# Optimization experiments

Hardware: AMD Instinct MI355X
Metric: run time of the kernel (lower is better)

Reference implementation:

```python
import jax, jax.numpy as jnp
import numpy as np

N = 100000          # nodes
E = 1600000         # edges (before self-loops)
F_IN = 128          # raw node features
TOPO = 8            # topological feature dim
HEADS1, HID1 = 8, 8 # conv1: 8 heads x 8 channels, concat -> 64
C_OUT = 40          # classes (conv2: 1 head, no concat)
NEG_SLOPE = 0.2     # PyG GATConv leaky_relu slope


def setup_inputs() -> dict:
    key = jax.random.key(0)
    ks = jax.random.split(key, 12)
    x = jax.random.normal(ks[0], (N, F_IN), jnp.float32)
    topo = jax.random.normal(ks[1], (N, TOPO), jnp.float32)
    edge_index = jax.random.randint(ks[2], (2, E), 0, N, jnp.int32)
    s = 0.1
    W1 = jax.random.normal(ks[3], (F_IN + TOPO, HEADS1 * HID1), jnp.float32) * s
    a_src1 = jax.random.normal(ks[4], (HEADS1, HID1), jnp.float32) * s
    a_dst1 = jax.random.normal(ks[5], (HEADS1, HID1), jnp.float32) * s
    b1 = jnp.zeros((HEADS1 * HID1,), jnp.float32)
    W2 = jax.random.normal(ks[6], (HEADS1 * HID1, C_OUT), jnp.float32) * s
    a_src2 = jax.random.normal(ks[7], (1, C_OUT), jnp.float32) * s
    a_dst2 = jax.random.normal(ks[8], (1, C_OUT), jnp.float32) * s
    b2 = jnp.zeros((C_OUT,), jnp.float32)
    return {"x": x, "topo": topo, "edge_index": edge_index,
            "W1": W1, "a_src1": a_src1, "a_dst1": a_dst1, "b1": b1,
            "W2": W2, "a_src2": a_src2, "a_dst2": a_dst2, "b2": b2}


def _gat_conv(x, src, dst, W, a_src, a_dst, b, heads, concat):
    # x: [N, Fin]; src/dst: [Etot] (self-loops already included)
    n = x.shape[0]
    h = (x @ W).reshape(n, heads, -1)                 # [N, H, C]
    alpha_s = jnp.sum(h * a_src[None], axis=-1)       # [N, H]
    alpha_d = jnp.sum(h * a_dst[None], axis=-1)       # [N, H]
    e = jax.nn.leaky_relu(alpha_s[src] + alpha_d[dst], NEG_SLOPE)  # [Etot, H]
    # segment softmax over destination nodes (numerically stable)
    m = jax.ops.segment_max(e, dst, num_segments=n)   # [N, H]
    ex = jnp.exp(e - m[dst])
    z = jax.ops.segment_sum(ex, dst, num_segments=n)  # [N, H]
    alpha = ex / (z[dst] + 1e-16)                     # [Etot, H]
    out = jax.ops.segment_sum(h[src] * alpha[..., None], dst, num_segments=n)  # [N,H,C]
    out = out.reshape(n, -1) if concat else out.mean(axis=1)
    return out + b


def reference(x, topo, edge_index, W1, a_src1, a_dst1, b1, W2, a_src2, a_dst2, b2):
    n = x.shape[0]
    loops = jnp.arange(n, dtype=edge_index.dtype)
    src = jnp.concatenate([edge_index[0], loops])  # PyG add_self_loops=True
    dst = jnp.concatenate([edge_index[1], loops])
    h = jnp.concatenate([x, topo], axis=1)         # [N, F_IN + TOPO]
    # dropout is identity in eval mode
    h = jax.nn.elu(_gat_conv(h, src, dst, W1, a_src1, a_dst1, b1, HEADS1, True))
    logits = _gat_conv(h, src, dst, W2, a_src2, a_dst2, b2, 1, False)
    return jax.nn.log_softmax(logits, axis=1)
```

## Files before the change

kernel.cpp:

```cpp
#include <hip/hip_runtime.h>
#include <math.h>


#define NBUK_MAX 512
#define BIN_CHUNK 4096
#define BUK_CAP 4608

typedef unsigned short ushort_t;

__device__ inline unsigned int f2bf(float f) {
    unsigned int u = __float_as_uint(f);
    u += 0x7FFFu + ((u >> 16) & 1u);
    return u >> 16;
}
__device__ inline float bf_lo(unsigned int u) {
    return __uint_as_float(u << 16);
}
__device__ inline float bf_hi(unsigned int u) {
    return __uint_as_float(u & 0xFFFF0000u);
}
__device__ inline float lrelu_exp(float q) {
    return __expf(q >= 0.f ? q : 0.2f * q);
}

__device__ inline int wave_incl_scan(int v, int lane) {
    #pragma unroll
    for (int ofs = 1; ofs < 64; ofs <<= 1) {
        int t = __shfl_up(v, ofs);
        if (lane >= ofs) v += t;
    }
    return v;
}

__global__ __launch_bounds__(256) void k_bin(const int* __restrict__ src,
                                             const int* __restrict__ dst,
                                             int* __restrict__ gCursor,
                                             unsigned int* __restrict__ tmp,
                                             int E, int NBUK) {
    __shared__ int lcnt[NBUK_MAX];
    __shared__ int lcur[NBUK_MAX];
    int tid = threadIdx.x;
    int base = blockIdx.x * BIN_CHUNK;
    for (int i = tid; i < NBUK; i += 256) lcnt[i] = 0;
    __syncthreads();
    int d[16];
    #pragma unroll
    for (int q = 0; q < 4; q++) {
        int e = base + q * 1024 + 4 * tid;
        if (e + 3 < E) {
            int4 v = *(const int4*)&dst[e];
            d[4 * q + 0] = v.x; d[4 * q + 1] = v.y;
            d[4 * q + 2] = v.z; d[4 * q + 3] = v.w;
        } else {
            #pragma unroll
            for (int k = 0; k < 4; k++)
                d[4 * q + k] = (e + k < E) ? dst[e + k] : -1;
        }
    }
    #pragma unroll
    for (int k = 0; k < 16; k++)
        if (d[k] >= 0) atomicAdd(&lcnt[d[k] >> 8], 1);
    __syncthreads();
    for (int b = tid; b < NBUK; b += 256) {
        int c = lcnt[b];
        lcur[b] = c ? b * BUK_CAP + atomicAdd(&gCursor[b], c) : 0;
    }
    __syncthreads();
    #pragma unroll
    for (int q = 0; q < 4; q++) {
        int e = base + q * 1024 + 4 * tid;
        int s[4];
        if (e + 3 < E) {
            int4 v = *(const int4*)&src[e];
            s[0] = v.x; s[1] = v.y; s[2] = v.z; s[3] = v.w;
        } else {
            #pragma unroll
            for (int k = 0; k < 4; k++)
                s[k] = (e + k < E) ? src[e + k] : 0;
        }
        #pragma unroll
        for (int k = 0; k < 4; k++) {
            int dd = d[4 * q + k];
            if (dd >= 0) {
                int p = atomicAdd(&lcur[dd >> 8], 1);
                tmp[p] = ((unsigned int)s[k] << 8) | (unsigned int)(dd & 255);
            }
        }
    }
}

__global__ __launch_bounds__(512) void k_fill2(const unsigned int* __restrict__ tmp,
                                               const int* __restrict__ gCursor,
                                               int* __restrict__ rowptr,
                                               int* __restrict__ rowEnd,
                                               int* __restrict__ csr, int N) {
    __shared__ int cnt[256];
    __shared__ int cur[256];
    __shared__ int wsum[4];
    int b = blockIdx.x, tid = threadIdx.x;
    int e0 = b * BUK_CAP;
    int cnt_e = gCursor[b];
    int e1 = e0 + cnt_e;
    if (tid < 256) cnt[tid] = 0;
    __syncthreads();
    {
        int nq = cnt_e >> 2;
        const uint4* t4 = (const uint4*)(tmp + e0);
        for (int q = tid; q < nq; q += 512) {
            uint4 v = t4[q];
            atomicAdd(&cnt[v.x & 255u], 1);
            atomicAdd(&cnt[v.y & 255u], 1);
            atomicAdd(&cnt[v.z & 255u], 1);
            atomicAdd(&cnt[v.w & 255u], 1);
        }
        for (int i = (nq << 2) + tid; i < cnt_e; i += 512)
            atomicAdd(&cnt[tmp[e0 + i] & 255u], 1);
    }
    __syncthreads();
    if (tid < 256) {
        int lane = tid & 63, wv = tid >> 6;
        int v = cnt[tid];
        int incl = wave_incl_scan(v, lane);
        if (lane == 63) wsum[wv] = incl;
        cnt[tid] = incl - v;
    }
    __syncthreads();
    if (tid < 256) {
        int wv = tid >> 6;
        int woff = 0;
        for (int i = 0; i < wv; i++) woff += wsum[i];
        int excl = woff + cnt[tid];
        int node = b * 256 + tid;
        int start = e0 + excl;
        cur[tid] = start;
        if (node < N) {
            rowptr[node] = start;
        }
    }
    __syncthreads();
    if (tid < 256) {
        int node = b * 256 + tid;
        if (node < N) rowEnd[node] = (tid < 255) ? cur[tid + 1] : e1;
    }
    __syncthreads();
    for (int i = e0 + tid; i < e1; i += 512) {
        unsigned int t = tmp[i];
        int p = atomicAdd(&cur[t & 255u], 1);
        csr[p] = (int)(t >> 8);
    }
}

__global__ __launch_bounds__(256) void k_xform1(const float* __restrict__ x,
                                                const float* __restrict__ topo,
                                                const float* __restrict__ W1,
                                                const float* __restrict__ asrc,
                                                const float* __restrict__ adst,
                                                ushort_t* __restrict__ h1b,
                                                float* __restrict__ as1,
                                                float* __restrict__ ad1, int N) {
    __shared__ float XT[136 * 64];
    __shared__ float WS[136 * 64];
    int tid = threadIdx.x;
    int n0 = blockIdx.x * 64;
    {
        const float4* W4 = (const float4*)W1;
        float4* WS4 = (float4*)WS;
        for (int i = tid; i < 2176; i += 256) WS4[i] = W4[i];
    }
    {
        const float4* x4 = (const float4*)x;
        for (int i = tid; i < 2048; i += 256) {
            int node = i & 63, k4 = i >> 6;
            int gn = n0 + node; if (gn > N - 1) gn = N - 1;
            float4 v = x4[(size_t)gn * 32 + k4];
            int k = k4 * 4;
            XT[(k + 0) * 64 + node] = v.x;
            XT[(k + 1) * 64 + node] = v.y;
            XT[(k + 2) * 64 + node] = v.z;
            XT[(k + 3) * 64 + node] = v.w;
        }
        const float4* t4 = (const float4*)topo;
        if (tid < 128) {
            int node = tid & 63, j4 = tid >> 6;
            int gn = n0 + node; if (gn > N - 1) gn = N - 1;
            float4 v = t4[(size_t)gn * 2 + j4];
            int k = 128 + j4 * 4;
            XT[(k + 0) * 64 + node] = v.x;
            XT[(k + 1) * 64 + node] = v.y;
            XT[(k + 2) * 64 + node] = v.z;
            XT[(k + 3) * 64 + node] = v.w;
        }
    }
    __syncthreads();
    int ci = tid & 15, ni = tid >> 4;
    int nb = ni * 4, cb = ci * 4;
    float acc[16];
    #pragma unroll
    for (int i = 0; i < 16; i++) acc[i] = 0.f;
    #pragma unroll 4
    for (int k = 0; k < 136; k++) {
        float4 xv = *(const float4*)&XT[k * 64 + nb];
        float4 wv = *(const float4*)&WS[k * 64 + cb];
        acc[0]  = fmaf(xv.x, wv.x, acc[0]);  acc[1]  = fmaf(xv.x, wv.y, acc[1]);
        acc[2]  = fmaf(xv.x, wv.z, acc[2]);  acc[3]  = fmaf(xv.x, wv.w, acc[3]);
        acc[4]  = fmaf(xv.y, wv.x, acc[4]);  acc[5]  = fmaf(xv.y, wv.y, acc[5]);
        acc[6]  = fmaf(xv.y, wv.z, acc[6]);  acc[7]  = fmaf(xv.y, wv.w, acc[7]);
        acc[8]  = fmaf(xv.z, wv.x, acc[8]);  acc[9]  = fmaf(xv.z, wv.y, acc[9]);
        acc[10] = fmaf(xv.z, wv.z, acc[10]); acc[11] = fmaf(xv.z, wv.w, acc[11]);
        acc[12] = fmaf(xv.w, wv.x, acc[12]); acc[13] = fmaf(xv.w, wv.y, acc[13]);
        acc[14] = fmaf(xv.w, wv.z, acc[14]); acc[15] = fmaf(xv.w, wv.w, acc[15]);
    }
    int head = cb >> 3;
    #pragma unroll
    for (int i = 0; i < 4; i++) {
        int n = n0 + nb + i;
        unsigned int p0 = f2bf(acc[i * 4 + 0]) | (f2bf(acc[i * 4 + 1]) << 16);
        unsigned int p1 = f2bf(acc[i * 4 + 2]) | (f2bf(acc[i * 4 + 3]) << 16);
        if (n < N) *(uint2*)&h1b[(size_t)n * 64 + cb] = make_uint2(p0, p1);
        float s = 0.f, d = 0.f;
        #pragma unroll
        for (int j = 0; j < 4; j++) {
            s = fmaf(acc[i * 4 + j], asrc[cb + j], s);
            d = fmaf(acc[i * 4 + j], adst[cb + j], d);
        }
        s += __shfl_xor(s, 1);
        d += __shfl_xor(d, 1);
        if ((ci & 1) == 0 && n < N) {
            as1[n * 8 + head] = s;
            ad1[n * 8 + head] = d;
        }
    }
}

#define AGG_FMA(W_, U_)                                           \
    {                                                             \
        acc[0] = fmaf(W_, bf_lo(U_.x), acc[0]);                   \
        acc[1] = fmaf(W_, bf_hi(U_.x), acc[1]);                   \
        acc[2] = fmaf(W_, bf_lo(U_.y), acc[2]);                   \
        acc[3] = fmaf(W_, bf_hi(U_.y), acc[3]);                   \
        acc[4] = fmaf(W_, bf_lo(U_.z), acc[4]);                   \
        acc[5] = fmaf(W_, bf_hi(U_.z), acc[5]);                   \
        acc[6] = fmaf(W_, bf_lo(U_.w), acc[6]);                   \
        acc[7] = fmaf(W_, bf_hi(U_.w), acc[7]);                   \
        z += W_;                                                  \
    }

__global__ __launch_bounds__(256) void k_agg1(const ushort_t* __restrict__ h1b,
                                              const float* __restrict__ as1,
                                              const float* __restrict__ ad1,
                                              const float* __restrict__ b1,
                                              const int* __restrict__ rowptr,
                                              const int* __restrict__ rowEnd,
                                              const int* __restrict__ csr,
                                              float* __restrict__ h2, int N) {
    int tid = threadIdx.x, lane = tid & 63;
    int n = blockIdx.x * 4 + (tid >> 6);
    if (n >= N) return;
    int g = lane >> 3;
    int head = lane & 7;
    const char* h1c = (const char*)h1b;
    unsigned hoff = (unsigned)head << 4;
    float adv = ad1[n * 8 + head];
    float acc[8];
    #pragma unroll
    for (int k = 0; k < 8; k++) acc[k] = 0.f;
    float z = 0.f;
    {
        float w = lrelu_exp(as1[n * 8 + head] + adv);
        if (g == 0) {
            uint4 u = *(const uint4*)(h1c + (((unsigned)n << 7) + hoff));
            acc[0] = w * bf_lo(u.x); acc[1] = w * bf_hi(u.x);
            acc[2] = w * bf_lo(u.y); acc[3] = w * bf_hi(u.y);
            acc[4] = w * bf_lo(u.z); acc[5] = w * bf_hi(u.z);
            acc[6] = w * bf_lo(u.w); acc[7] = w * bf_hi(u.w);
            z = w;
        }
    }
    int j = rowptr[n], j1 = rowEnd[n];
    for (; j + 16 <= j1; j += 16) {
        int cv = csr[j + (lane & 15)];
        int se0 = __shfl(cv, g);
        int se1 = __shfl(cv, 8 + g);
        float av0 = as1[se0 * 8 + head];
        float av1 = as1[se1 * 8 + head];
        uint4 u0 = *(const uint4*)(h1c + (((unsigned)se0 << 7) + hoff));
        uint4 u1 = *(const uint4*)(h1c + (((unsigned)se1 << 7) + hoff));
        float w0 = lrelu_exp(av0 + adv);
        float w1 = lrelu_exp(av1 + adv);
        AGG_FMA(w0, u0);
        AGG_FMA(w1, u1);
    }
    if (j + 8 <= j1) {
        int cv = csr[j + (lane & 7)];
        int se = __shfl(cv, g);
        float av = as1[se * 8 + head];
        uint4 u = *(const uint4*)(h1c + (((unsigned)se << 7) + hoff));
        float w = lrelu_exp(av + adv);
        AGG_FMA(w, u);
        j += 8;
    }
    int t = j1 - j;
    if (t > 0) {
        int idx = (lane & 7); idx = idx < t ? idx : t - 1;
        int cv = csr[j + idx];
        int ge = g < t ? g : t - 1;
        int se = __shfl(cv, ge);
        float w = (g < t) ? lrelu_exp(as1[se * 8 + head] + adv) : 0.f;
        uint4 u = *(const uint4*)(h1c + (((unsigned)se << 7) + hoff));
        AGG_FMA(w, u);
    }
    #pragma unroll
    for (int k = 0; k < 8; k++) {
        acc[k] += __shfl_xor(acc[k], 8);
        acc[k] += __shfl_xor(acc[k], 16);
        acc[k] += __shfl_xor(acc[k], 32);
    }
    z += __shfl_xor(z, 8); z += __shfl_xor(z, 16); z += __shfl_xor(z, 32);
    if (g == 0) {
        float inv = 1.f / (z + 1e-16f);
        float o[8];
        #pragma unroll
        for (int k = 0; k < 8; k++) {
            float v = acc[k] * inv + b1[head * 8 + k];
            o[k] = v > 0.f ? v : (__expf(v) - 1.f);
        }
        float4* dp = (float4*)&h2[(size_t)n * 64 + head * 8];
        dp[0] = make_float4(o[0], o[1], o[2], o[3]);
        dp[1] = make_float4(o[4], o[5], o[6], o[7]);
    }
}

__global__ __launch_bounds__(256) void k_xform2(const float* __restrict__ h2,
                                                const float* __restrict__ W2,
                                                const float* __restrict__ asrc2,
                                                const float* __restrict__ adst2,
                                                ushort_t* __restrict__ gb,
                                                float* __restrict__ as2,
                                                float* __restrict__ ad2, int N) {
    __shared__ float XT[64 * 64];
    __shared__ float WS[64 * 40];
    int tid = threadIdx.x;
    int n0 = blockIdx.x * 64;
    {
        const float4* W4 = (const float4*)W2;
        float4* WS4 = (float4*)WS;
        for (int i = tid; i < 640; i += 256) WS4[i] = W4[i];
    }
    {
        const float4* h4 = (const float4*)h2;
        for (int i = tid; i < 1024; i += 256) {
            int node = i & 63, k4 = i >> 6;
            int gn = n0 + node; if (gn > N - 1) gn = N - 1;
            float4 v = h4[(size_t)gn * 16 + k4];
            int k = k4 * 4;
            XT[(k + 0) * 64 + node] = v.x;
            XT[(k + 1) * 64 + node] = v.y;
            XT[(k + 2) * 64 + node] = v.z;
            XT[(k + 3) * 64 + node] = v.w;
        }
    }
    __syncthreads();
    int ci = tid & 15, ni = tid >> 4;
    int nb = ni * 4, cb = ci * 4;
    float acc[16];
    #pragma unroll
    for (int i = 0; i < 16; i++) acc[i] = 0.f;
    if (ci < 10) {
        #pragma unroll 4
        for (int k = 0; k < 64; k++) {
            float4 xv = *(const float4*)&XT[k * 64 + nb];
            float4 wv = *(const float4*)&WS[k * 40 + cb];
            acc[0]  = fmaf(xv.x, wv.x, acc[0]);  acc[1]  = fmaf(xv.x, wv.y, acc[1]);
            acc[2]  = fmaf(xv.x, wv.z, acc[2]);  acc[3]  = fmaf(xv.x, wv.w, acc[3]);
            acc[4]  = fmaf(xv.y, wv.x, acc[4]);  acc[5]  = fmaf(xv.y, wv.y, acc[5]);
            acc[6]  = fmaf(xv.y, wv.z, acc[6]);  acc[7]  = fmaf(xv.y, wv.w, acc[7]);
            acc[8]  = fmaf(xv.z, wv.x, acc[8]);  acc[9]  = fmaf(xv.z, wv.y, acc[9]);
            acc[10] = fmaf(xv.z, wv.z, acc[10]); acc[11] = fmaf(xv.z, wv.w, acc[11]);
            acc[12] = fmaf(xv.w, wv.x, acc[12]); acc[13] = fmaf(xv.w, wv.y, acc[13]);
            acc[14] = fmaf(xv.w, wv.z, acc[14]); acc[15] = fmaf(xv.w, wv.w, acc[15]);
        }
    }
    #pragma unroll
    for (int i = 0; i < 4; i++) {
        int n = n0 + nb + i;
        if (ci < 10 && n < N) {
            unsigned int p0 = f2bf(acc[i * 4 + 0]) | (f2bf(acc[i * 4 + 1]) << 16);
            unsigned int p1 = f2bf(acc[i * 4 + 2]) | (f2bf(acc[i * 4 + 3]) << 16);
            *(uint2*)&gb[(size_t)n * 64 + cb] = make_uint2(p0, p1);
        }
        float s = 0.f, d = 0.f;
        if (ci < 10) {
            #pragma unroll
            for (int j = 0; j < 4; j++) {
                s = fmaf(acc[i * 4 + j], asrc2[cb + j], s);
                d = fmaf(acc[i * 4 + j], adst2[cb + j], d);
            }
        }
        s += __shfl_xor(s, 1); s += __shfl_xor(s, 2);
        s += __shfl_xor(s, 4); s += __shfl_xor(s, 8);
        d += __shfl_xor(d, 1); d += __shfl_xor(d, 2);
        d += __shfl_xor(d, 4); d += __shfl_xor(d, 8);
        if (ci == 0 && n < N) { as2[n] = s; ad2[n] = d; }
    }
}

__global__ __launch_bounds__(256) void k_agg2(const ushort_t* __restrict__ gb,
                                              const float* __restrict__ as2,
                                              const float* __restrict__ ad2,
                                              const float* __restrict__ b2,
                                              const int* __restrict__ rowptr,
                                              const int* __restrict__ rowEnd,
                                              const int* __restrict__ csr,
                                              float* __restrict__ out, int N) {
    int tid = threadIdx.x, lane = tid & 63;
    int n = blockIdx.x * 4 + (tid >> 6);
    if (n >= N) return;
    int g = lane >> 3;
    int p = lane & 7;
    const char* gbc = (const char*)gb;
    unsigned poff = (unsigned)p << 4;
    float add = ad2[n];
    float acc[8];
    #pragma unroll
    for (int k = 0; k < 8; k++) acc[k] = 0.f;
    float z = 0.f;
    {
        float w = lrelu_exp(as2[n] + add);
        if (g == 0) {
            uint4 u = *(const uint4*)(gbc + (((unsigned)n << 7) + poff));
            acc[0] = w * bf_lo(u.x); acc[1] = w * bf_hi(u.x);
            acc[2] = w * bf_lo(u.y); acc[3] = w * bf_hi(u.y);
            acc[4] = w * bf_lo(u.z); acc[5] = w * bf_hi(u.z);
            acc[6] = w * bf_lo(u.w); acc[7] = w * bf_hi(u.w);
            z = w;
        }
    }
    int j = rowptr[n], j1 = rowEnd[n];
    for (; j + 16 <= j1; j += 16) {
        int cv = csr[j + (lane & 15)];
        int se0 = __shfl(cv, g);
        int se1 = __shfl(cv, 8 + g);
        float av0 = as2[se0];
        float av1 = as2[se1];
        uint4 u0 = *(const uint4*)(gbc + (((unsigned)se0 << 7) + poff));
        uint4 u1 = *(const uint4*)(gbc + (((unsigned)se1 << 7) + poff));
        float w0 = lrelu_exp(av0 + add);
        float w1 = lrelu_exp(av1 + add);
        AGG_FMA(w0, u0);
        AGG_FMA(w1, u1);
    }
    if (j + 8 <= j1) {
        int cv = csr[j + (lane & 7)];
        int se = __shfl(cv, g);
        float av = as2[se];
        uint4 u = *(const uint4*)(gbc + (((unsigned)se << 7) + poff));
        float w = lrelu_exp(av + add);
        AGG_FMA(w, u);
        j += 8;
    }
    int t = j1 - j;
    if (t > 0) {
        int idx = (lane & 7); idx = idx < t ? idx : t - 1;
        int cv = csr[j + idx];
        int ge = g < t ? g : t - 1;
        int se = __shfl(cv, ge);
        float w = (g < t) ? lrelu_exp(as2[se] + add) : 0.f;
        uint4 u = *(const uint4*)(gbc + (((unsigned)se << 7) + poff));
        AGG_FMA(w, u);
    }
    #pragma unroll
    for (int k = 0; k < 8; k++) {
        acc[k] += __shfl_xor(acc[k], 8);
        acc[k] += __shfl_xor(acc[k], 16);
        acc[k] += __shfl_xor(acc[k], 32);
    }
    z += __shfl_xor(z, 8); z += __shfl_xor(z, 16); z += __shfl_xor(z, 32);
    if (g == 0) {
        bool act = (p < 5);
        float inv = 1.f / (z + 1e-16f);
        float l[8];
        float mv = -INFINITY;
        if (act) {
            #pragma unroll
            for (int k = 0; k < 8; k++) {
                l[k] = acc[k] * inv + b2[p * 8 + k];
                mv = fmaxf(mv, l[k]);
            }
        }
        mv = fmaxf(mv, __shfl_xor(mv, 1));
        mv = fmaxf(mv, __shfl_xor(mv, 2));
        mv = fmaxf(mv, __shfl_xor(mv, 4));
        float ev = 0.f;
        if (act) {
            #pragma unroll
            for (int k = 0; k < 8; k++) ev += __expf(l[k] - mv);
        }
        ev += __shfl_xor(ev, 1);
        ev += __shfl_xor(ev, 2);
        ev += __shfl_xor(ev, 4);
        if (act) {
            float ls = mv + __logf(ev);
            float4* dp = (float4*)&out[(size_t)n * 40 + p * 8];
            dp[0] = make_float4(l[0] - ls, l[1] - ls, l[2] - ls, l[3] - ls);
            dp[1] = make_float4(l[4] - ls, l[5] - ls, l[6] - ls, l[7] - ls);
        }
    }
}

extern "C" void kernel_launch(void* const* d_in, const int* in_sizes, int n_in,
                              void* d_out, int out_size, void* d_ws, size_t ws_size,
                              hipStream_t stream) {
    const float* x    = (const float*)d_in[0];
    const float* topo = (const float*)d_in[1];
    const int*   ei   = (const int*)d_in[2];
    const float* W1   = (const float*)d_in[3];
    const float* a_s1 = (const float*)d_in[4];
    const float* a_d1 = (const float*)d_in[5];
    const float* b1   = (const float*)d_in[6];
    const float* W2   = (const float*)d_in[7];
    const float* a_s2 = (const float*)d_in[8];
    const float* a_d2 = (const float*)d_in[9];
    const float* b2   = (const float*)d_in[10];
    float* out = (float*)d_out;

    int N = in_sizes[0] / 128;
    int E = in_sizes[2] / 2;
    const int* esrc = ei;
    const int* edst = ei + E;
    int NBUK = (N + 255) / 256;
    size_t cap = (size_t)NBUK * BUK_CAP;

    char* ws = (char*)d_ws;
    size_t off = 0;
    auto alloc = [&](size_t bytes) -> void* {
        void* p = ws + off;
        off = (off + bytes + 255) & ~(size_t)255;
        return p;
    };
    ushort_t* h1b  = (ushort_t*)alloc((size_t)N * 64 * 2);
    float* as1     = (float*)alloc((size_t)N * 8 * 4);
    float* ad1     = (float*)alloc((size_t)N * 8 * 4);
    float* h2      = (float*)alloc((size_t)N * 64 * 4);
    ushort_t* gb   = (ushort_t*)alloc((size_t)N * 64 * 2);
    float* as2     = (float*)alloc((size_t)N * 4);
    float* ad2     = (float*)alloc((size_t)N * 4);
    int*   rowptr  = (int*)alloc((size_t)N * 4);
    int*   rowEnd  = (int*)alloc((size_t)N * 4);
    int*   csr     = (int*)alloc(cap * 4);
    unsigned int* tmp = (unsigned int*)alloc(cap * 4);
    int* gCursor   = (int*)alloc((size_t)NBUK * 4);

    hipMemsetAsync(gCursor, 0, (size_t)NBUK * 4, stream);
    int nbin = (E + BIN_CHUNK - 1) / BIN_CHUNK;
    k_bin<<<nbin, 256, 0, stream>>>(esrc, edst, gCursor, tmp, E, NBUK);
    k_fill2<<<NBUK, 512, 0, stream>>>(tmp, gCursor, rowptr, rowEnd, csr, N);

    int nbg = (N + 63) / 64;
    int nb4 = (N + 3) / 4;
    k_xform1<<<nbg, 256, 0, stream>>>(x, topo, W1, a_s1, a_d1, h1b, as1, ad1, N);
    k_agg1<<<nb4, 256, 0, stream>>>(h1b, as1, ad1, b1, rowptr, rowEnd, csr, h2, N);
    k_xform2<<<nbg, 256, 0, stream>>>(h2, W2, a_s2, a_d2, gb, as2, ad2, N);
    k_agg2<<<nb4, 256, 0, stream>>>(gb, as2, ad2, b2, rowptr, rowEnd, csr, out, N);
}
```

Baseline: 314.5 us.

## Compact layer-2 bf16 features to 40-wide rows and remap aggregation lanes

```diff
diff --git a/kernel.cpp b/kernel.cpp
--- a/kernel.cpp
+++ b/kernel.cpp
@@ -386,7 +386,7 @@
         if (ci < 10 && n < N) {
             unsigned int p0 = f2bf(acc[i * 4 + 0]) | (f2bf(acc[i * 4 + 1]) << 16);
             unsigned int p1 = f2bf(acc[i * 4 + 2]) | (f2bf(acc[i * 4 + 3]) << 16);
-            *(uint2*)&gb[(size_t)n * 64 + cb] = make_uint2(p0, p1);
+            *(uint2*)&gb[(size_t)n * 40 + cb] = make_uint2(p0, p1);
         }
         float s = 0.f, d = 0.f;
         if (ci < 10) {
@@ -415,10 +415,11 @@
     int tid = threadIdx.x, lane = tid & 63;
     int n = blockIdx.x * 4 + (tid >> 6);
     if (n >= N) return;
-    int g = lane >> 3;
-    int p = lane & 7;
+    int g = lane / 5; if (g > 11) g = 11;
+    int p = lane - g * 5; if (p > 4) p = 4;
     const char* gbc = (const char*)gb;
     unsigned poff = (unsigned)p << 4;
+    int lm12 = lane % 12;
     float add = ad2[n];
     float acc[8];
     #pragma unroll
@@ -427,7 +428,7 @@
     {
         float w = lrelu_exp(as2[n] + add);
         if (g == 0) {
-            uint4 u = *(const uint4*)(gbc + (((unsigned)n << 7) + poff));
+            uint4 u = *(const uint4*)(gbc + ((unsigned)n * 80u + poff));
             acc[0] = w * bf_lo(u.x); acc[1] = w * bf_hi(u.x);
             acc[2] = w * bf_lo(u.y); acc[3] = w * bf_hi(u.y);
             acc[4] = w * bf_lo(u.z); acc[5] = w * bf_hi(u.z);
@@ -436,74 +437,81 @@
         }
     }
     int j = rowptr[n], j1 = rowEnd[n];
-    for (; j + 16 <= j1; j += 16) {
-        int cv = csr[j + (lane & 15)];
-        int se0 = __shfl(cv, g);
-        int se1 = __shfl(cv, 8 + g);
+    for (; j + 24 <= j1; j += 24) {
+        int cv0 = csr[j + lm12];
+        int cv1 = csr[j + 12 + lm12];
+        int se0 = __shfl(cv0, g);
+        int se1 = __shfl(cv1, g);
         float av0 = as2[se0];
         float av1 = as2[se1];
-        uint4 u0 = *(const uint4*)(gbc + (((unsigned)se0 << 7) + poff));
-        uint4 u1 = *(const uint4*)(gbc + (((unsigned)se1 << 7) + poff));
+        uint4 u0 = *(const uint4*)(gbc + ((unsigned)se0 * 80u + poff));
+        uint4 u1 = *(const uint4*)(gbc + ((unsigned)se1 * 80u + poff));
         float w0 = lrelu_exp(av0 + add);
         float w1 = lrelu_exp(av1 + add);
         AGG_FMA(w0, u0);
         AGG_FMA(w1, u1);
     }
-    if (j + 8 <= j1) {
-        int cv = csr[j + (lane & 7)];
+    if (j + 12 <= j1) {
+        int cv = csr[j + lm12];
         int se = __shfl(cv, g);
         float av = as2[se];
-        uint4 u = *(const uint4*)(gbc + (((unsigned)se << 7) + poff));
+        uint4 u = *(const uint4*)(gbc + ((unsigned)se * 80u + poff));
         float w = lrelu_exp(av + add);
         AGG_FMA(w, u);
-        j += 8;
+        j += 12;
     }
     int t = j1 - j;
     if (t > 0) {
-        int idx = (lane & 7); idx = idx < t ? idx : t - 1;
+        int idx = lm12 < t ? lm12 : t - 1;
         int cv = csr[j + idx];
         int ge = g < t ? g : t - 1;
         int se = __shfl(cv, ge);
         float w = (g < t) ? lrelu_exp(as2[se] + add) : 0.f;
-        uint4 u = *(const uint4*)(gbc + (((unsigned)se << 7) + poff));
+        uint4 u = *(const uint4*)(gbc + ((unsigned)se * 80u + poff));
         AGG_FMA(w, u);
     }
     #pragma unroll
     for (int k = 0; k < 8; k++) {
-        acc[k] += __shfl_xor(acc[k], 8);
-        acc[k] += __shfl_xor(acc[k], 16);
-        acc[k] += __shfl_xor(acc[k], 32);
-    }
-    z += __shfl_xor(z, 8); z += __shfl_xor(z, 16); z += __shfl_xor(z, 32);
-    if (g == 0) {
-        bool act = (p < 5);
+        float v = acc[k];
+        v += __shfl(v, lane + 30);
+        v += __shfl(v, lane + 15);
+        v += __shfl(v, lane + 5) + __shfl(v, lane + 10);
+        acc[k] = v;
+    }
+    {
+        float v = z;
+        v += __shfl(v, lane + 30);
+        v += __shfl(v, lane + 15);
+        v += __shfl(v, lane + 5) + __shfl(v, lane + 10);
+        z = v;
+    }
+    bool act = (lane < 5);
+    float l[8];
+    float mv = -INFINITY;
+    if (act) {
         float inv = 1.f / (z + 1e-16f);
-        float l[8];
-        float mv = -INFINITY;
-        if (act) {
-            #pragma unroll
-            for (int k = 0; k < 8; k++) {
-                l[k] = acc[k] * inv + b2[p * 8 + k];
-                mv = fmaxf(mv, l[k]);
-            }
-        }
-        mv = fmaxf(mv, __shfl_xor(mv, 1));
-        mv = fmaxf(mv, __shfl_xor(mv, 2));
-        mv = fmaxf(mv, __shfl_xor(mv, 4));
-        float ev = 0.f;
-        if (act) {
-            #pragma unroll
-            for (int k = 0; k < 8; k++) ev += __expf(l[k] - mv);
-        }
-        ev += __shfl_xor(ev, 1);
-        ev += __shfl_xor(ev, 2);
-        ev += __shfl_xor(ev, 4);
-        if (act) {
-            float ls = mv + __logf(ev);
-            float4* dp = (float4*)&out[(size_t)n * 40 + p * 8];
-            dp[0] = make_float4(l[0] - ls, l[1] - ls, l[2] - ls, l[3] - ls);
-            dp[1] = make_float4(l[4] - ls, l[5] - ls, l[6] - ls, l[7] - ls);
-        }
+        #pragma unroll
+        for (int k = 0; k < 8; k++) {
+            l[k] = acc[k] * inv + b2[lane * 8 + k];
+            mv = fmaxf(mv, l[k]);
+        }
+    }
+    mv = fmaxf(mv, __shfl_xor(mv, 1));
+    mv = fmaxf(mv, __shfl_xor(mv, 2));
+    mv = fmaxf(mv, __shfl_xor(mv, 4));
+    float ev = 0.f;
+    if (act) {
+        #pragma unroll
+        for (int k = 0; k < 8; k++) ev += __expf(l[k] - mv);
+    }
+    ev += __shfl_xor(ev, 1);
+    ev += __shfl_xor(ev, 2);
+    ev += __shfl_xor(ev, 4);
+    if (act) {
+        float ls = mv + __logf(ev);
+        float4* dp = (float4*)&out[(size_t)n * 40 + lane * 8];
+        dp[0] = make_float4(l[0] - ls, l[1] - ls, l[2] - ls, l[3] - ls);
+        dp[1] = make_float4(l[4] - ls, l[5] - ls, l[6] - ls, l[7] - ls);
     }
 }
 
@@ -541,7 +549,7 @@
     float* as1     = (float*)alloc((size_t)N * 8 * 4);
     float* ad1     = (float*)alloc((size_t)N * 8 * 4);
     float* h2      = (float*)alloc((size_t)N * 64 * 4);
-    ushort_t* gb   = (ushort_t*)alloc((size_t)N * 64 * 2);
+    ushort_t* gb   = (ushort_t*)alloc((size_t)N * 40 * 2);
     float* as2     = (float*)alloc((size_t)N * 4);
     float* ad2     = (float*)alloc((size_t)N * 4);
     int*   rowptr  = (int*)alloc((size_t)N * 4);
```

After: 316.4 us. Within noise of the previous version (+0.6%).
